# Performance work log

Measured on AMD Instinct MI355X. Metric: run time of the kernel, lower is better.

Reference implementation:

```python
import jax, jax.numpy as jnp
import numpy as np

N = 100_000          # nodes
E = 1_600_000        # directed edges (before self-loops)
IN_DIM, H1, H2, H3 = 128, 64, 64, 64
NEG_SLOPE = 0.2      # PyG GATConv default


def setup_inputs() -> dict:
    key = jax.random.key(0)
    ks = jax.random.split(key, 20)

    def glorot(k, shape):
        fan = shape[0] + shape[-1] if len(shape) > 1 else 1 + shape[0]
        return jax.random.normal(k, shape, jnp.float32) * np.float32(np.sqrt(2.0 / fan))

    inp = {
        "x": jax.random.normal(ks[0], (N, IN_DIM), jnp.float32),
        "edge_index": jax.random.randint(ks[1], (2, E), 0, N, jnp.int32),
        "W1": glorot(ks[2], (IN_DIM, H1)), "a1s": glorot(ks[3], (H1,)), "a1d": glorot(ks[4], (H1,)), "b1": jnp.zeros((H1,), jnp.float32),
        "W2": glorot(ks[5], (H1, H2)),     "a2s": glorot(ks[6], (H2,)), "a2d": glorot(ks[7], (H2,)), "b2": jnp.zeros((H2,), jnp.float32),
        "W3": glorot(ks[8], (H2, H3)),     "a3s": glorot(ks[9], (H3,)), "a3d": glorot(ks[10], (H3,)), "b3": jnp.zeros((H3,), jnp.float32),
        "Wl": glorot(ks[11], (H3, 1)),     "bl": jnp.zeros((1,), jnp.float32),
    }
    return inp


def _gat_layer(x, src, dst, W, a_src, a_dst, b):
    # x: [N, Fin]; src/dst: [E'] (self-loops included)
    h = x @ W                              # [N, Fout]
    alpha_s = h @ a_src                    # [N]
    alpha_d = h @ a_dst                    # [N]
    e = jax.nn.leaky_relu(alpha_s[src] + alpha_d[dst], NEG_SLOPE)  # [E']
    # segment softmax over edges grouped by destination node
    m = jax.ops.segment_max(e, dst, num_segments=N)
    p = jnp.exp(e - m[dst])
    s = jax.ops.segment_sum(p, dst, num_segments=N)
    alpha = p / (s[dst] + 1e-16)           # [E']
    out = jax.ops.segment_sum(alpha[:, None] * h[src], dst, num_segments=N)  # [N, Fout]
    return out + b


def reference(x, edge_index, W1, a1s, a1d, b1, W2, a2s, a2d, b2, W3, a3s, a3d, b3, Wl, bl):
    # add self-loops (PyG GATConv default add_self_loops=True)
    loops = jnp.arange(N, dtype=edge_index.dtype)
    src = jnp.concatenate([edge_index[0], loops])
    dst = jnp.concatenate([edge_index[1], loops])

    h = jax.nn.relu(_gat_layer(x, src, dst, W1, a1s, a1d, b1))   # dropout is identity in eval
    h = jax.nn.relu(_gat_layer(h, src, dst, W2, a2s, a2d, b2))
    h = jax.nn.relu(_gat_layer(h, src, dst, W3, a3s, a3d, b3))
    return jax.nn.sigmoid(h @ Wl + bl)      # [N, 1]
```

## Files before the change

kernel.cpp:

```cpp
#include <hip/hip_runtime.h>
#include <hip/hip_bf16.h>
#include <math.h>

#define BSH 8
#define MAXBK 512
#define PCHUNK 4096
#define BCSR_CAP 6144

typedef __attribute__((ext_vector_type(8)))  short short8;
typedef __attribute__((ext_vector_type(16))) float f32x16;

__device__ __forceinline__ float half_reduce_max(float v) {
  #pragma unroll
  for (int off = 16; off; off >>= 1) v = fmaxf(v, __shfl_xor(v, off));
  return v;
}
__device__ __forceinline__ float half_reduce_sum(float v) {
  #pragma unroll
  for (int off = 16; off; off >>= 1) v += __shfl_xor(v, off);
  return v;
}

__device__ __forceinline__ unsigned f2bf(float f) {
  unsigned u = __float_as_uint(f);
  return (u + 0x7fffu + ((u >> 16) & 1u)) >> 16;
}
__device__ __forceinline__ float bf_lo(unsigned u) { return __uint_as_float(u << 16); }
__device__ __forceinline__ float bf_hi(unsigned u) { return __uint_as_float(u & 0xffff0000u); }

__device__ __forceinline__ void async_copy16(const void* gsrc, void* ldst) {
  __builtin_amdgcn_global_load_lds(
      (const __attribute__((address_space(1))) void*)gsrc,
      (__attribute__((address_space(3))) void*)ldst, 16, 0, 0);
}

__device__ __forceinline__ void wave0_excl_scan(unsigned* arr, unsigned* out, int n, int t) {
  if (t < 64) {
    unsigned carry = 0;
    for (int c = 0; c < n / 64; c++) {
      unsigned v = arr[c * 64 + t];
      unsigned s = v;
      #pragma unroll
      for (int off = 1; off < 64; off <<= 1) {
        unsigned u = __shfl_up(s, off);
        if ((t & 63) >= off) s += u;
      }
      out[c * 64 + t] = s - v + carry;
      carry += __shfl(s, 63);
    }
  }
}


__global__ __launch_bounds__(256) void k_bhist(const int* __restrict__ ei,
                                               unsigned* __restrict__ gbucket,
                                               int E, int nbk) {
  __shared__ unsigned hist[MAXBK];
  int t = threadIdx.x;
  for (int i = t; i < nbk; i += 256) hist[i] = 0;
  __syncthreads();
  const int4* d4 = (const int4*)(ei + E);
  int nd4 = E >> 2;
  for (int i = blockIdx.x * 256 + t; i < nd4; i += gridDim.x * 256) {
    int4 d = d4[i];
    atomicAdd(&hist[d.x >> BSH], 1u);
    atomicAdd(&hist[d.y >> BSH], 1u);
    atomicAdd(&hist[d.z >> BSH], 1u);
    atomicAdd(&hist[d.w >> BSH], 1u);
  }
  if (blockIdx.x == 0) {
    for (int e = (nd4 << 2) + t; e < E; e += 256)
      atomicAdd(&hist[ei[E + e] >> BSH], 1u);
  }
  __syncthreads();
  for (int i = t; i < nbk; i += 256)
    if (hist[i]) atomicAdd(&gbucket[i], hist[i]);
}

__global__ __launch_bounds__(256) void k_bscan(const unsigned* __restrict__ gbucket,
                                               unsigned* __restrict__ bbase,
                                               unsigned* __restrict__ bfill,
                                               int nbk, int EE, int Nn) {
  __shared__ unsigned arr[MAXBK], exc[MAXBK];
  int t = threadIdx.x;
  for (int i = t; i < MAXBK; i += 256) {
    unsigned v = 0;
    if (i < nbk) {
      int rem = Nn - (i << BSH);
      unsigned sl = rem >= 256 ? 256u : (unsigned)(rem > 0 ? rem : 0);
      v = gbucket[i] + sl;
    }
    arr[i] = v;
  }
  __syncthreads();
  wave0_excl_scan(arr, exc, MAXBK, t);
  __syncthreads();
  for (int i = t; i < nbk; i += 256) { bbase[i] = exc[i]; bfill[i] = exc[i]; }
  if (t == 0) bbase[nbk] = (unsigned)EE;
}

__global__ __launch_bounds__(256) void k_part(const int* __restrict__ ei,
                                              unsigned* __restrict__ bfill,
                                              uint2* __restrict__ part,
                                              int E, int EE) {
  __shared__ uint2 stage[PCHUNK];
  __shared__ unsigned lcnt[MAXBK], lexcl[MAXBK], lbase[MAXBK];
  int t = threadIdx.x;
  int base = blockIdx.x * PCHUNK;
  int cnt = EE - base; if (cnt > PCHUNK) cnt = PCHUNK;
  for (int i = t; i < MAXBK; i += 256) lcnt[i] = 0;
  __syncthreads();

  uint2 ed[16]; unsigned loc[16];
  #pragma unroll
  for (int i = 0; i < 16; i++) {
    int e = base + i * 256 + t;
    if (e < EE) {
      int s, d;
      if (e < E) { s = ei[e]; d = ei[E + e]; } else { s = e - E; d = s; }
      ed[i] = make_uint2((unsigned)s, (unsigned)d);
      loc[i] = atomicAdd(&lcnt[(unsigned)d >> BSH], 1u);
    }
  }
  __syncthreads();
  wave0_excl_scan(lcnt, lexcl, MAXBK, t);
  __syncthreads();
  for (int i = t; i < MAXBK; i += 256) {
    unsigned c = lcnt[i];
    lbase[i] = c ? atomicAdd(&bfill[i], c) : 0u;
  }
  __syncthreads();
  #pragma unroll
  for (int i = 0; i < 16; i++) {
    int e = base + i * 256 + t;
    if (e < EE) stage[lexcl[ed[i].y >> BSH] + loc[i]] = ed[i];
  }
  __syncthreads();
  for (int i = t; i < cnt; i += 256) {
    uint2 v = stage[i];
    unsigned b = v.y >> BSH;
    part[lbase[b] + ((unsigned)i - lexcl[b])] = v;
  }
}

__global__ __launch_bounds__(256) void k_bcsr(const uint2* __restrict__ part,
                                              const unsigned* __restrict__ bbase,
                                              int* __restrict__ rowptr,
                                              int* __restrict__ csr_src,
                                              int Nn, int nbk) {
  __shared__ unsigned sdeg[256], sexcl[256], sfill[256];
  __shared__ uint2 epart[BCSR_CAP];
  int t = threadIdx.x, b = blockIdx.x;
  int e0 = (int)bbase[b], e1 = (int)bbase[b + 1];
  int cnt = e1 - e0;
  bool fits = cnt <= BCSR_CAP;
  sdeg[t] = 0; sfill[t] = 0;
  __syncthreads();
  if (fits) {
    for (int j = t; j < cnt; j += 256) {
      uint2 v = part[e0 + j];
      epart[j] = v;
      atomicAdd(&sdeg[v.y & 255u], 1u);
    }
  } else {
    for (int j = e0 + t; j < e1; j += 256)
      atomicAdd(&sdeg[part[j].y & 255u], 1u);
  }
  __syncthreads();
  wave0_excl_scan(sdeg, sexcl, 256, t);
  __syncthreads();
  int node = (b << BSH) + t;
  if (node < Nn) rowptr[node] = e0 + (int)sexcl[t];
  if (b == nbk - 1 && t == 0) rowptr[Nn] = e1;
  if (fits) {
    for (int j = t; j < cnt; j += 256) {
      uint2 v = epart[j];
      unsigned dl = v.y & 255u;
      unsigned k = atomicAdd(&sfill[dl], 1u);
      csr_src[e0 + (int)sexcl[dl] + (int)k] = (int)v.x;
    }
  } else {
    for (int j = e0 + t; j < e1; j += 256) {
      uint2 v = part[j];
      unsigned dl = v.y & 255u;
      unsigned k = atomicAdd(&sfill[dl], 1u);
      csr_src[e0 + (int)sexcl[dl] + (int)k] = (int)v.x;
    }
  }
}


__global__ __launch_bounds__(256) void k_wprep(const float* __restrict__ W1,
                                               const float* __restrict__ W2,
                                               const float* __restrict__ W3,
                                               short8* __restrict__ wf) {
  int idx = blockIdx.x * 256 + threadIdx.x;
  if (idx >= 2048) return;
  int g = idx >> 6, l = idx & 63;
  const float* W; int s, t;
  if (g < 16)      { W = W1; s = g >> 1;        t = g & 1; }
  else if (g < 24) { W = W2; s = (g - 16) >> 1; t = g & 1; }
  else             { W = W3; s = (g - 24) >> 1; t = g & 1; }
  int of = t * 32 + (l & 31);
  int k0 = s * 16 + (l >> 5) * 8;
  short8 v;
  #pragma unroll
  for (int e = 0; e < 8; e++) v[e] = (short)f2bf(W[(k0 + e) * 64 + of]);
  wf[idx] = v;
}


template <int K, bool F32IN>
__global__ __launch_bounds__(256) void k_gemm7(
    const void* __restrict__ xin, const short8* __restrict__ wf,
    const float* __restrict__ avs, const float* __restrict__ avd,
    unsigned* __restrict__ h, float* __restrict__ as_out,
    float* __restrict__ ad_out, int Nn) {
  constexpr int NS = K / 16;
  constexpr int RB = F32IN ? K * 4 : K * 2;
  constexpr int RSH = F32IN ? (K == 128 ? 9 : 8) : (K == 128 ? 8 : 7);
  __shared__ __align__(16) char xs_raw[128 * RB];
  int t = threadIdx.x, lane = t & 63, wid = t >> 6;
  int l31 = lane & 31, hi = lane >> 5;

  short8 wa[NS * 2];
  #pragma unroll
  for (int i = 0; i < NS * 2; i++) wa[i] = wf[i * 64 + lane];

  int tile0 = blockIdx.x * 128;
  const char* xg = (const char*)xin;
  constexpr int CH = (128 * RB) / (256 * 16);
  #pragma unroll
  for (int i = 0; i < CH; i++) {
    int off = (i * 256 + t) * 16;
    int row = off >> RSH;
    int inrow = off & (RB - 1);
    long grow = (long)tile0 + row;
    if (grow > (long)Nn - 1) grow = Nn - 1;
    async_copy16(xg + grow * RB + (inrow ^ ((row & 7) << 4)), xs_raw + off);
  }
  __syncthreads();

  f32x16 acc0 = {0,0,0,0,0,0,0,0,0,0,0,0,0,0,0,0};
  f32x16 acc1 = {0,0,0,0,0,0,0,0,0,0,0,0,0,0,0,0};
  int rowl = wid * 32 + l31;
  int swz = (rowl & 7) << 4;

  #pragma unroll
  for (int s = 0; s < NS; s++) {
    short8 bf;
    if constexpr (F32IN) {
      int ph = (rowl * RB + s * 64 + hi * 32) ^ swz;
      float4 fA = *(const float4*)(xs_raw + ph);
      float4 fB = *(const float4*)(xs_raw + (ph ^ 16));
      bf[0] = (short)f2bf(fA.x); bf[1] = (short)f2bf(fA.y);
      bf[2] = (short)f2bf(fA.z); bf[3] = (short)f2bf(fA.w);
      bf[4] = (short)f2bf(fB.x); bf[5] = (short)f2bf(fB.y);
      bf[6] = (short)f2bf(fB.z); bf[7] = (short)f2bf(fB.w);
    } else {
      int ph = (rowl * RB + s * 32 + hi * 16) ^ swz;
      bf = *(const short8*)(xs_raw + ph);
    }
    acc0 = __builtin_amdgcn_mfma_f32_32x32x16_bf16(wa[2 * s], bf, acc0, 0, 0, 0);
    acc1 = __builtin_amdgcn_mfma_f32_32x32x16_bf16(wa[2 * s + 1], bf, acc1, 0, 0, 0);
  }

  int xrow = tile0 + rowl;
  bool ok = xrow < Nn;
  float asp = 0.f, adp = 0.f;
  #pragma unroll
  for (int r = 0; r < 16; r += 2) {
    int rof = (r & 3) + 8 * (r >> 2);
    int of0 = rof + 4 * hi;
    if (ok) {
      h[(size_t)xrow * 32 + (of0 >> 1)] =
          (f2bf(acc0[r + 1]) << 16) | f2bf(acc0[r]);
      h[(size_t)xrow * 32 + 16 + (of0 >> 1)] =
          (f2bf(acc1[r + 1]) << 16) | f2bf(acc1[r]);
    }
    asp += acc0[r] * avs[of0] + acc0[r + 1] * avs[of0 + 1]
         + acc1[r] * avs[of0 + 32] + acc1[r + 1] * avs[of0 + 33];
    adp += acc0[r] * avd[of0] + acc0[r + 1] * avd[of0 + 1]
         + acc1[r] * avd[of0 + 32] + acc1[r + 1] * avd[of0 + 33];
  }
  asp += __shfl_xor(asp, 32);
  adp += __shfl_xor(adp, 32);
  if (ok && hi == 0) { as_out[xrow] = asp; ad_out[xrow] = adp; }
}


template <int FINAL>
__global__ __launch_bounds__(256) void k_agg9(
    const int* __restrict__ rowptr, const int* __restrict__ csr_src,
    const unsigned* __restrict__ hp, const float* __restrict__ as_,
    const float* __restrict__ ad_, const float* __restrict__ bias,
    unsigned* __restrict__ out, const float* __restrict__ Wlin,
    const float* __restrict__ blin, float* __restrict__ fout, int Nn) {
  __shared__ float2 psbuf[4][2][32];
  int t = threadIdx.x, lane = t & 63, wid = t >> 6;
  int fl = lane & 31, hh = lane >> 5;
  int n = blockIdx.x * 8 + wid * 2 + hh;
  bool valid = n < Nn;
  int nn = valid ? n : (Nn - 1);
  int r0 = rowptr[nn], r1 = rowptr[nn + 1];
  int deg = valid ? (r1 - r0) : 0;
  float ad = ad_[nn];

  if (deg <= 32) {
    int src = (fl < deg) ? csr_src[r0 + fl] : 0;
    float e = (fl < deg) ? (as_[src] + ad) : -3.0e38f;
    e = (e >= 0.f) ? e : 0.2f * e;
    float m = half_reduce_max(e);
    float p = (fl < deg) ? __expf(e - m) : 0.f;
    float inv = 1.f / (half_reduce_sum(p) + 1e-16f);
    psbuf[wid][hh][fl] = make_float2(p, __uint_as_float((unsigned)src * 128u));

    int sub = fl >> 4, q = fl & 15;
    const char* hq = (const char*)hp + q * 8;
    const float2* psb = psbuf[wid][hh];
    float a0 = 0.f, a1 = 0.f, a2 = 0.f, a3 = 0.f;
    float b0 = 0.f, b1 = 0.f, b2 = 0.f, b3 = 0.f;

    float2 ps0 = psb[sub];
    float2 ps1 = psb[2 + sub];
    uint2 v0 = *(const uint2*)(hq + __float_as_uint(ps0.y));
    uint2 v1 = *(const uint2*)(hq + __float_as_uint(ps1.y));
    for (int jj = 4; jj < deg; jj += 4) {
      float2 nps0 = psb[jj + sub];
      float2 nps1 = psb[jj + 2 + sub];
      uint2 nv0 = *(const uint2*)(hq + __float_as_uint(nps0.y));
      uint2 nv1 = *(const uint2*)(hq + __float_as_uint(nps1.y));
      a0 = fmaf(ps0.x, bf_lo(v0.x), a0);
      a1 = fmaf(ps0.x, bf_hi(v0.x), a1);
      a2 = fmaf(ps0.x, bf_lo(v0.y), a2);
      a3 = fmaf(ps0.x, bf_hi(v0.y), a3);
      b0 = fmaf(ps1.x, bf_lo(v1.x), b0);
      b1 = fmaf(ps1.x, bf_hi(v1.x), b1);
      b2 = fmaf(ps1.x, bf_lo(v1.y), b2);
      b3 = fmaf(ps1.x, bf_hi(v1.y), b3);
      ps0 = nps0; ps1 = nps1; v0 = nv0; v1 = nv1;
    }
    a0 = fmaf(ps0.x, bf_lo(v0.x), a0);
    a1 = fmaf(ps0.x, bf_hi(v0.x), a1);
    a2 = fmaf(ps0.x, bf_lo(v0.y), a2);
    a3 = fmaf(ps0.x, bf_hi(v0.y), a3);
    b0 = fmaf(ps1.x, bf_lo(v1.x), b0);
    b1 = fmaf(ps1.x, bf_hi(v1.x), b1);
    b2 = fmaf(ps1.x, bf_lo(v1.y), b2);
    b3 = fmaf(ps1.x, bf_hi(v1.y), b3);

    a0 += b0; a1 += b1; a2 += b2; a3 += b3;
    a0 += __shfl_xor(a0, 16);
    a1 += __shfl_xor(a1, 16);
    a2 += __shfl_xor(a2, 16);
    a3 += __shfl_xor(a3, 16);

    float4 bi = ((const float4*)bias)[q];
    float o0 = fmaxf(fmaf(a0, inv, bi.x), 0.f);
    float o1 = fmaxf(fmaf(a1, inv, bi.y), 0.f);
    float o2 = fmaxf(fmaf(a2, inv, bi.z), 0.f);
    float o3 = fmaxf(fmaf(a3, inv, bi.w), 0.f);
    if (FINAL) {
      float4 wl = ((const float4*)Wlin)[q];
      float rv = (sub == 0) ? (o0 * wl.x + o1 * wl.y + o2 * wl.z + o3 * wl.w) : 0.f;
      rv = half_reduce_sum(rv);
      if (valid && fl == 0) {
        float z = rv + blin[0];
        fout[n] = 1.f / (1.f + __expf(-z));
      }
    } else if (valid && sub == 0) {
      uint2 pk;
      pk.x = (f2bf(o1) << 16) | f2bf(o0);
      pk.y = (f2bf(o3) << 16) | f2bf(o2);
      *(uint2*)(out + (size_t)n * 32 + 2 * q) = pk;
    }
  } else {
    float acc0 = 0.f, acc1 = 0.f;
    float m = -3.0e38f;
    for (int j = r0 + fl; j < r1; j += 32) {
      float e = as_[csr_src[j]] + ad;
      e = (e >= 0.f) ? e : 0.2f * e;
      m = fmaxf(m, e);
    }
    m = half_reduce_max(m);
    float ssum = 0.f;
    for (int j = r0; j < r1; ++j) {
      int src = csr_src[j];
      float e = as_[src] + ad;
      e = (e >= 0.f) ? e : 0.2f * e;
      float p = __expf(e - m);
      ssum += p;
      unsigned v = hp[(size_t)src * 32 + fl];
      acc0 = fmaf(p, bf_lo(v), acc0);
      acc1 = fmaf(p, bf_hi(v), acc1);
    }
    float inv2 = 1.f / (ssum + 1e-16f);
    acc0 *= inv2;
    acc1 *= inv2;
    float2 bi = ((const float2*)bias)[fl];
    float o0 = fmaxf(acc0 + bi.x, 0.f);
    float o1 = fmaxf(acc1 + bi.y, 0.f);
    if (FINAL) {
      float2 wl = ((const float2*)Wlin)[fl];
      float rv = half_reduce_sum(o0 * wl.x + o1 * wl.y);
      if (valid && fl == 0) {
        float z = rv + blin[0];
        fout[n] = 1.f / (1.f + __expf(-z));
      }
    } else {
      if (valid) out[(size_t)n * 32 + fl] = (f2bf(o1) << 16) | f2bf(o0);
    }
  }
}

extern "C" void kernel_launch(void* const* d_in, const int* in_sizes, int n_in,
                              void* d_out, int out_size, void* d_ws, size_t ws_size,
                              hipStream_t stream) {
  const float* x   = (const float*)d_in[0];
  const int*   ei  = (const int*)d_in[1];
  const float* W1  = (const float*)d_in[2];
  const float* a1s = (const float*)d_in[3];
  const float* a1d = (const float*)d_in[4];
  const float* b1  = (const float*)d_in[5];
  const float* W2  = (const float*)d_in[6];
  const float* a2s = (const float*)d_in[7];
  const float* a2d = (const float*)d_in[8];
  const float* b2  = (const float*)d_in[9];
  const float* W3  = (const float*)d_in[10];
  const float* a3s = (const float*)d_in[11];
  const float* a3d = (const float*)d_in[12];
  const float* b3  = (const float*)d_in[13];
  const float* Wl  = (const float*)d_in[14];
  const float* bl  = (const float*)d_in[15];

  const int N  = in_sizes[0] / 128;
  const int E  = in_sizes[1] / 2;
  const int EE = E + N;
  const int nbk = (N + 255) >> 8;

  char* p = (char*)d_ws;
  auto alloc = [&](size_t bytes) { char* r = p; p += (bytes + 255) & ~(size_t)255; return r; };
  unsigned* gbucket = (unsigned*)alloc((size_t)MAXBK * 4);
  unsigned* bbase   = (unsigned*)alloc((size_t)(MAXBK + 1) * 4);
  unsigned* bfill   = (unsigned*)alloc((size_t)MAXBK * 4);
  short8*   wf      = (short8*)alloc(2048 * 16);
  int*      rowptr  = (int*)alloc((size_t)(N + 1) * 4);
  int*      csr_src = (int*)alloc((size_t)EE * 4);
  unsigned* hbuf    = (unsigned*)alloc((size_t)N * 32 * 4);
  char*     regionA = alloc((size_t)EE * 8);
  float*    as_     = (float*)alloc((size_t)N * 4);
  float*    ad_     = (float*)alloc((size_t)N * 4);

  uint2*    part = (uint2*)regionA;
  unsigned* obuf = (unsigned*)regionA;

  hipMemsetAsync(gbucket, 0, (size_t)MAXBK * 4, stream);

  k_wprep<<<8, 256, 0, stream>>>(W1, W2, W3, wf);
  k_bhist<<<256, 256, 0, stream>>>(ei, gbucket, E, nbk);
  k_bscan<<<1, 256, 0, stream>>>(gbucket, bbase, bfill, nbk, EE, N);
  k_part<<<(EE + PCHUNK - 1) / PCHUNK, 256, 0, stream>>>(ei, bfill, part, E, EE);
  k_bcsr<<<nbk, 256, 0, stream>>>(part, bbase, rowptr, csr_src, N, nbk);

  int gb = (N + 127) / 128;
  int nb = (N + 7) / 8;

  k_gemm7<128, true><<<gb, 256, 0, stream>>>(x, wf, a1s, a1d, hbuf, as_, ad_, N);
  k_agg9<0><<<nb, 256, 0, stream>>>(rowptr, csr_src, hbuf, as_, ad_, b1, obuf,
                                    nullptr, nullptr, nullptr, N);
  k_gemm7<64, false><<<gb, 256, 0, stream>>>(obuf, wf + 16 * 64, a2s, a2d,
                                             hbuf, as_, ad_, N);
  k_agg9<0><<<nb, 256, 0, stream>>>(rowptr, csr_src, hbuf, as_, ad_, b2, obuf,
                                    nullptr, nullptr, nullptr, N);
  k_gemm7<64, false><<<gb, 256, 0, stream>>>(obuf, wf + 24 * 64, a3s, a3d,
                                             hbuf, as_, ad_, N);
  k_agg9<1><<<nb, 256, 0, stream>>>(rowptr, csr_src, hbuf, as_, ad_, b3, nullptr,
                                    Wl, bl, (float*)d_out, N);
}
```

Baseline: 252.4 us.

## Make GEMM persistent with double-buffered tiles; fully unroll aggregation gathers

The projection GEMM becomes a persistent kernel. Each 128-thread block walks several 64-row tiles and async-prefetches the next tile into a second shared buffer while computing the current one. This is meant to hide global load latency and cut launch and block setup overhead. Separately, the low-degree aggregation path now issues all up to 8 gather iterations' loads up front into registers before the FMAs, to raise memory-level parallelism. The cost is higher register pressure and guarded unrolled code.

```diff
diff --git a/kernel.cpp b/kernel.cpp
--- a/kernel.cpp
+++ b/kernel.cpp
@@ -211,15 +211,15 @@
 
 
 template <int K, bool F32IN>
-__global__ __launch_bounds__(256) void k_gemm7(
+__global__ __launch_bounds__(128) void k_gemm8(
     const void* __restrict__ xin, const short8* __restrict__ wf,
     const float* __restrict__ avs, const float* __restrict__ avd,
     unsigned* __restrict__ h, float* __restrict__ as_out,
-    float* __restrict__ ad_out, int Nn) {
+    float* __restrict__ ad_out, int Nn, int ntiles) {
   constexpr int NS = K / 16;
   constexpr int RB = F32IN ? K * 4 : K * 2;
-  constexpr int RSH = F32IN ? (K == 128 ? 9 : 8) : (K == 128 ? 8 : 7);
-  __shared__ __align__(16) char xs_raw[128 * RB];
+  constexpr int RSH = F32IN ? 9 : (K == 128 ? 8 : 7);
+  __shared__ __align__(16) char xs[2][64 * RB];
   int t = threadIdx.x, lane = t & 63, wid = t >> 6;
   int l31 = lane & 31, hi = lane >> 5;
 
@@ -227,70 +227,86 @@
   #pragma unroll
   for (int i = 0; i < NS * 2; i++) wa[i] = wf[i * 64 + lane];
 
-  int tile0 = blockIdx.x * 128;
   const char* xg = (const char*)xin;
-  constexpr int CH = (128 * RB) / (256 * 16);
-  #pragma unroll
-  for (int i = 0; i < CH; i++) {
-    int off = (i * 256 + t) * 16;
-    int row = off >> RSH;
-    int inrow = off & (RB - 1);
-    long grow = (long)tile0 + row;
-    if (grow > (long)Nn - 1) grow = Nn - 1;
-    async_copy16(xg + grow * RB + (inrow ^ ((row & 7) << 4)), xs_raw + off);
-  }
-  __syncthreads();
-
-  f32x16 acc0 = {0,0,0,0,0,0,0,0,0,0,0,0,0,0,0,0};
-  f32x16 acc1 = {0,0,0,0,0,0,0,0,0,0,0,0,0,0,0,0};
-  int rowl = wid * 32 + l31;
-  int swz = (rowl & 7) << 4;
-
-  #pragma unroll
-  for (int s = 0; s < NS; s++) {
-    short8 bf;
-    if constexpr (F32IN) {
-      int ph = (rowl * RB + s * 64 + hi * 32) ^ swz;
-      float4 fA = *(const float4*)(xs_raw + ph);
-      float4 fB = *(const float4*)(xs_raw + (ph ^ 16));
-      bf[0] = (short)f2bf(fA.x); bf[1] = (short)f2bf(fA.y);
-      bf[2] = (short)f2bf(fA.z); bf[3] = (short)f2bf(fA.w);
-      bf[4] = (short)f2bf(fB.x); bf[5] = (short)f2bf(fB.y);
-      bf[6] = (short)f2bf(fB.z); bf[7] = (short)f2bf(fB.w);
-    } else {
-      int ph = (rowl * RB + s * 32 + hi * 16) ^ swz;
-      bf = *(const short8*)(xs_raw + ph);
-    }
-    acc0 = __builtin_amdgcn_mfma_f32_32x32x16_bf16(wa[2 * s], bf, acc0, 0, 0, 0);
-    acc1 = __builtin_amdgcn_mfma_f32_32x32x16_bf16(wa[2 * s + 1], bf, acc1, 0, 0, 0);
-  }
-
-  int xrow = tile0 + rowl;
-  bool ok = xrow < Nn;
-  float asp = 0.f, adp = 0.f;
-  #pragma unroll
-  for (int r = 0; r < 16; r += 2) {
-    int rof = (r & 3) + 8 * (r >> 2);
-    int of0 = rof + 4 * hi;
-    if (ok) {
-      h[(size_t)xrow * 32 + (of0 >> 1)] =
-          (f2bf(acc0[r + 1]) << 16) | f2bf(acc0[r]);
-      h[(size_t)xrow * 32 + 16 + (of0 >> 1)] =
-          (f2bf(acc1[r + 1]) << 16) | f2bf(acc1[r]);
-    }
-    asp += acc0[r] * avs[of0] + acc0[r + 1] * avs[of0 + 1]
-         + acc1[r] * avs[of0 + 32] + acc1[r + 1] * avs[of0 + 33];
-    adp += acc0[r] * avd[of0] + acc0[r + 1] * avd[of0 + 1]
-         + acc1[r] * avd[of0 + 32] + acc1[r + 1] * avd[of0 + 33];
-  }
-  asp += __shfl_xor(asp, 32);
-  adp += __shfl_xor(adp, 32);
-  if (ok && hi == 0) { as_out[xrow] = asp; ad_out[xrow] = adp; }
+  auto stage = [&](int buf, int tl) {
+    constexpr int CH = (64 * RB) / (128 * 16);
+    #pragma unroll
+    for (int i = 0; i < CH; i++) {
+      int off = (i * 128 + t) * 16;
+      int row = off >> RSH;
+      int inrow = off & (RB - 1);
+      long grow = (long)tl * 64 + row;
+      if (grow > (long)Nn - 1) grow = Nn - 1;
+      async_copy16(xg + grow * RB + (inrow ^ ((row & 7) << 4)), xs[buf] + off);
+    }
+  };
+
+  int tile = blockIdx.x;
+  if (tile >= ntiles) return;
+  stage(0, tile);
+  __syncthreads();
+  int buf = 0;
+
+  while (tile < ntiles) {
+    int nxt = tile + gridDim.x;
+    if (nxt < ntiles) stage(buf ^ 1, nxt);
+
+    f32x16 acc0 = {0,0,0,0,0,0,0,0,0,0,0,0,0,0,0,0};
+    f32x16 acc1 = {0,0,0,0,0,0,0,0,0,0,0,0,0,0,0,0};
+    int rowl = wid * 32 + l31;
+    int swz = (rowl & 7) << 4;
+    const char* xb = xs[buf];
+
+    #pragma unroll
+    for (int s = 0; s < NS; s++) {
+      short8 bf;
+      if constexpr (F32IN) {
+        int ph = (rowl * RB + s * 64 + hi * 32) ^ swz;
+        float4 fA = *(const float4*)(xb + ph);
+        float4 fB = *(const float4*)(xb + (ph ^ 16));
+        bf[0] = (short)f2bf(fA.x); bf[1] = (short)f2bf(fA.y);
+        bf[2] = (short)f2bf(fA.z); bf[3] = (short)f2bf(fA.w);
+        bf[4] = (short)f2bf(fB.x); bf[5] = (short)f2bf(fB.y);
+        bf[6] = (short)f2bf(fB.z); bf[7] = (short)f2bf(fB.w);
+      } else {
+        int ph = (rowl * RB + s * 32 + hi * 16) ^ swz;
+        bf = *(const short8*)(xb + ph);
+      }
+      acc0 = __builtin_amdgcn_mfma_f32_32x32x16_bf16(wa[2 * s], bf, acc0, 0, 0, 0);
+      acc1 = __builtin_amdgcn_mfma_f32_32x32x16_bf16(wa[2 * s + 1], bf, acc1, 0, 0, 0);
+    }
+
+    int xrow = tile * 64 + rowl;
+    bool ok = xrow < Nn;
+    float asp = 0.f, adp = 0.f;
+    #pragma unroll
+    for (int r = 0; r < 16; r += 2) {
+      int rof = (r & 3) + 8 * (r >> 2);
+      int of0 = rof + 4 * hi;
+      if (ok) {
+        h[(size_t)xrow * 32 + (of0 >> 1)] =
+            (f2bf(acc0[r + 1]) << 16) | f2bf(acc0[r]);
+        h[(size_t)xrow * 32 + 16 + (of0 >> 1)] =
+            (f2bf(acc1[r + 1]) << 16) | f2bf(acc1[r]);
+      }
+      asp += acc0[r] * avs[of0] + acc0[r + 1] * avs[of0 + 1]
+           + acc1[r] * avs[of0 + 32] + acc1[r + 1] * avs[of0 + 33];
+      adp += acc0[r] * avd[of0] + acc0[r + 1] * avd[of0 + 1]
+           + acc1[r] * avd[of0 + 32] + acc1[r + 1] * avd[of0 + 33];
+    }
+    asp += __shfl_xor(asp, 32);
+    adp += __shfl_xor(adp, 32);
+    if (ok && hi == 0) { as_out[xrow] = asp; ad_out[xrow] = adp; }
+
+    __syncthreads();
+    buf ^= 1;
+    tile = nxt;
+  }
 }
 
 
 template <int FINAL>
-__global__ __launch_bounds__(256) void k_agg9(
+__global__ __launch_bounds__(256) void k_agg10(
     const int* __restrict__ rowptr, const int* __restrict__ csr_src,
     const unsigned* __restrict__ hp, const float* __restrict__ as_,
     const float* __restrict__ ad_, const float* __restrict__ bias,
@@ -318,37 +334,35 @@
     int sub = fl >> 4, q = fl & 15;
     const char* hq = (const char*)hp + q * 8;
     const float2* psb = psbuf[wid][hh];
+
+    float pp0[8], pp1[8];
+    uint2 vv0[8], vv1[8];
+    #pragma unroll
+    for (int it = 0; it < 8; it++) {
+      if (it * 4 < deg) {
+        float2 ps0 = psb[it * 4 + sub];
+        float2 ps1 = psb[it * 4 + 2 + sub];
+        pp0[it] = ps0.x;
+        pp1[it] = ps1.x;
+        vv0[it] = *(const uint2*)(hq + __float_as_uint(ps0.y));
+        vv1[it] = *(const uint2*)(hq + __float_as_uint(ps1.y));
+      }
+    }
     float a0 = 0.f, a1 = 0.f, a2 = 0.f, a3 = 0.f;
     float b0 = 0.f, b1 = 0.f, b2 = 0.f, b3 = 0.f;
-
-    float2 ps0 = psb[sub];
-    float2 ps1 = psb[2 + sub];
-    uint2 v0 = *(const uint2*)(hq + __float_as_uint(ps0.y));
-    uint2 v1 = *(const uint2*)(hq + __float_as_uint(ps1.y));
-    for (int jj = 4; jj < deg; jj += 4) {
-      float2 nps0 = psb[jj + sub];
-      float2 nps1 = psb[jj + 2 + sub];
-      uint2 nv0 = *(const uint2*)(hq + __float_as_uint(nps0.y));
-      uint2 nv1 = *(const uint2*)(hq + __float_as_uint(nps1.y));
-      a0 = fmaf(ps0.x, bf_lo(v0.x), a0);
-      a1 = fmaf(ps0.x, bf_hi(v0.x), a1);
-      a2 = fmaf(ps0.x, bf_lo(v0.y), a2);
-      a3 = fmaf(ps0.x, bf_hi(v0.y), a3);
-      b0 = fmaf(ps1.x, bf_lo(v1.x), b0);
-      b1 = fmaf(ps1.x, bf_hi(v1.x), b1);
-      b2 = fmaf(ps1.x, bf_lo(v1.y), b2);
-      b3 = fmaf(ps1.x, bf_hi(v1.y), b3);
-      ps0 = nps0; ps1 = nps1; v0 = nv0; v1 = nv1;
-    }
-    a0 = fmaf(ps0.x, bf_lo(v0.x), a0);
-    a1 = fmaf(ps0.x, bf_hi(v0.x), a1);
-    a2 = fmaf(ps0.x, bf_lo(v0.y), a2);
-    a3 = fmaf(ps0.x, bf_hi(v0.y), a3);
-    b0 = fmaf(ps1.x, bf_lo(v1.x), b0);
-    b1 = fmaf(ps1.x, bf_hi(v1.x), b1);
-    b2 = fmaf(ps1.x, bf_lo(v1.y), b2);
-    b3 = fmaf(ps1.x, bf_hi(v1.y), b3);
-
+    #pragma unroll
+    for (int it = 0; it < 8; it++) {
+      if (it * 4 < deg) {
+        a0 = fmaf(pp0[it], bf_lo(vv0[it].x), a0);
+        a1 = fmaf(pp0[it], bf_hi(vv0[it].x), a1);
+        a2 = fmaf(pp0[it], bf_lo(vv0[it].y), a2);
+        a3 = fmaf(pp0[it], bf_hi(vv0[it].y), a3);
+        b0 = fmaf(pp1[it], bf_lo(vv1[it].x), b0);
+        b1 = fmaf(pp1[it], bf_hi(vv1[it].x), b1);
+        b2 = fmaf(pp1[it], bf_lo(vv1[it].y), b2);
+        b3 = fmaf(pp1[it], bf_hi(vv1[it].y), b3);
+      }
+    }
     a0 += b0; a1 += b1; a2 += b2; a3 += b3;
     a0 += __shfl_xor(a0, 16);
     a1 += __shfl_xor(a1, 16);
@@ -462,18 +476,20 @@
   k_part<<<(EE + PCHUNK - 1) / PCHUNK, 256, 0, stream>>>(ei, bfill, part, E, EE);
   k_bcsr<<<nbk, 256, 0, stream>>>(part, bbase, rowptr, csr_src, N, nbk);
 
-  int gb = (N + 127) / 128;
+  int ntile64 = (N + 63) / 64;
+  int g1 = ntile64 < 512 ? ntile64 : 512;
+  int g2 = ntile64 < 768 ? ntile64 : 768;
   int nb = (N + 7) / 8;
 
-  k_gemm7<128, true><<<gb, 256, 0, stream>>>(x, wf, a1s, a1d, hbuf, as_, ad_, N);
-  k_agg9<0><<<nb, 256, 0, stream>>>(rowptr, csr_src, hbuf, as_, ad_, b1, obuf,
-                                    nullptr, nullptr, nullptr, N);
-  k_gemm7<64, false><<<gb, 256, 0, stream>>>(obuf, wf + 16 * 64, a2s, a2d,
-                                             hbuf, as_, ad_, N);
-  k_agg9<0><<<nb, 256, 0, stream>>>(rowptr, csr_src, hbuf, as_, ad_, b2, obuf,
-                                    nullptr, nullptr, nullptr, N);
-  k_gemm7<64, false><<<gb, 256, 0, stream>>>(obuf, wf + 24 * 64, a3s, a3d,
-                                             hbuf, as_, ad_, N);
-  k_agg9<1><<<nb, 256, 0, stream>>>(rowptr, csr_src, hbuf, as_, ad_, b3, nullptr,
-                                    Wl, bl, (float*)d_out, N);
-}
+  k_gemm8<128, true><<<g1, 128, 0, stream>>>(x, wf, a1s, a1d, hbuf, as_, ad_, N, ntile64);
+  k_agg10<0><<<nb, 256, 0, stream>>>(rowptr, csr_src, hbuf, as_, ad_, b1, obuf,
+                                     nullptr, nullptr, nullptr, N);
+  k_gemm8<64, false><<<g2, 128, 0, stream>>>(obuf, wf + 16 * 64, a2s, a2d,
+                                             hbuf, as_, ad_, N, ntile64);
+  k_agg10<0><<<nb, 256, 0, stream>>>(rowptr, csr_src, hbuf, as_, ad_, b2, obuf,
+                                     nullptr, nullptr, nullptr, N);
+  k_gemm8<64, false><<<g2, 128, 0, stream>>>(obuf, wf + 24 * 64, a3s, a3d,
+                                             hbuf, as_, ad_, N, ntile64);
+  k_agg10<1><<<nb, 256, 0, stream>>>(rowptr, csr_src, hbuf, as_, ad_, b3, nullptr,
+                                     Wl, bl, (float*)d_out, N);
+}
```

New measurement: 240.5 us. -4.7%, faster.
